# Kernel tuning notes

Hardware: AMD Instinct MI355X
Metric: run time of the kernel (lower is better)

## Reference

```python
import jax, jax.numpy as jnp
import numpy as np

N_NODES = 100000
N_EDGES = 1200000
IN_DIM, HID_DIM, LAT_DIM = 128, 64, 32


def gcn_conv(x, W, b, src, dst, n_nodes):
    # PyG GCNConv with add_self_loops=True, symmetric normalization.
    # src/dst already include self loops.
    h = x @ W  # [N, out]
    deg = jax.ops.segment_sum(jnp.ones_like(dst, dtype=h.dtype), dst,
                              num_segments=n_nodes)  # includes self loop -> >=1
    dinv = jax.lax.rsqrt(deg)
    norm = dinv[src] * dinv[dst]  # [E]
    msg = h[src] * norm[:, None]  # gather + scale, [E, out]
    out = jax.ops.segment_sum(msg, dst, num_segments=n_nodes)  # scatter-add
    return out + b


def setup_inputs() -> dict:
    key = jax.random.key(0)
    ks = jax.random.split(key, 9)
    x = jax.random.normal(ks[0], (N_NODES, IN_DIM), dtype=jnp.float32)
    edge_index = jax.random.randint(ks[1], (2, N_EDGES), 0, N_NODES, dtype=jnp.int32)
    s1 = 1.0 / np.sqrt(IN_DIM)
    s2 = 1.0 / np.sqrt(HID_DIM)
    W1 = jax.random.uniform(ks[2], (IN_DIM, HID_DIM), jnp.float32, -s1, s1)
    b1 = jnp.zeros((HID_DIM,), jnp.float32)
    Wm = jax.random.uniform(ks[3], (HID_DIM, LAT_DIM), jnp.float32, -s2, s2)
    bm = jnp.zeros((LAT_DIM,), jnp.float32)
    Wv = jax.random.uniform(ks[4], (HID_DIM, LAT_DIM), jnp.float32, -s2, s2)
    bv = jnp.zeros((LAT_DIM,), jnp.float32)
    noise = jax.random.normal(ks[5], (N_NODES, LAT_DIM), dtype=jnp.float32)
    return {"x": x, "edge_index": edge_index, "W1": W1, "b1": b1,
            "Wm": Wm, "bm": bm, "Wv": Wv, "bv": bv, "noise": noise}


def reference(x, edge_index, W1, b1, Wm, bm, Wv, bv, noise):
    n = x.shape[0]
    loops = jnp.arange(n, dtype=edge_index.dtype)
    src = jnp.concatenate([edge_index[0], loops])
    dst = jnp.concatenate([edge_index[1], loops])
    h = jnp.tanh(gcn_conv(x, W1, b1, src, dst, n))
    mean = gcn_conv(h, Wm, bm, src, dst, n)
    logvar = gcn_conv(h, Wv, bv, src, dst, n)
    z = noise * jnp.exp(0.5 * logvar) + mean
    return (z, mean, logvar)
```

## Files before the change

### kernel.cpp

```cpp
#include <hip/hip_runtime.h>
#include <math.h>

#define TILE 4096
#define CSHIFT 11
#define CMASK 2047
#define NCMAX 64

typedef __attribute__((ext_vector_type(8))) short bf16x8;
typedef __attribute__((ext_vector_type(4))) float f32x4;


__device__ __forceinline__ unsigned int pack_bf16(float a, float b) {
  unsigned int ua = __float_as_uint(a);
  ua += 0x7FFFu + ((ua >> 16) & 1u);
  unsigned int ub = __float_as_uint(b);
  ub += 0x7FFFu + ((ub >> 16) & 1u);
  return (ua >> 16) | (ub & 0xFFFF0000u);
}

__device__ __forceinline__ void add8(float* acc, uint4 hv) {
  unsigned int u[4] = {hv.x, hv.y, hv.z, hv.w};
#pragma unroll
  for (int i = 0; i < 4; ++i) {
    acc[2 * i]     += __uint_as_float(u[i] << 16);
    acc[2 * i + 1] += __uint_as_float(u[i] & 0xFFFF0000u);
  }
}

__device__ __forceinline__ void fma4(float4& acc, float s, const float4& w) {
  acc.x = fmaf(s, w.x, acc.x);
  acc.y = fmaf(s, w.y, acc.y);
  acc.z = fmaf(s, w.z, acc.z);
  acc.w = fmaf(s, w.w, acc.w);
}


__global__ void zero_kernel(int* __restrict__ p, int n) {
  int i = blockIdx.x * blockDim.x + threadIdx.x;
  if (i < n) p[i] = 0;
}

__global__ __launch_bounds__(256) void coarse_hist_kernel(const int* __restrict__ dst,
    int* __restrict__ ccnt, int e) {
  __shared__ int h[NCMAX];
  if (threadIdx.x < NCMAX) h[threadIdx.x] = 0;
  __syncthreads();
  for (int i = blockIdx.x * 256 + threadIdx.x; i < e; i += gridDim.x * 256)
    atomicAdd(&h[dst[i] >> CSHIFT], 1);
  __syncthreads();
  if (threadIdx.x < NCMAX && h[threadIdx.x])
    atomicAdd(&ccnt[threadIdx.x * 16], h[threadIdx.x]);
}

__global__ __launch_bounds__(64) void coarse_scan_kernel(const int* __restrict__ ccnt,
    int* __restrict__ coff, int* __restrict__ ccur, int* __restrict__ off,
    int nc, int n, int e) {
  int t = threadIdx.x;
  int v = (t < nc) ? ccnt[t * 16] : 0;
  int incl = v;
#pragma unroll
  for (int ofs = 1; ofs < 64; ofs <<= 1) {
    int w = __shfl_up(incl, ofs);
    if (t >= ofs) incl += w;
  }
  int excl = incl - v;
  if (t < nc) { coff[t] = excl; ccur[t * 16] = excl; }
  if (t == nc - 1) coff[nc] = incl;
  if (t == 0) off[n] = e;
}

__global__ __launch_bounds__(256) void coarse_partition_kernel(const int* __restrict__ src,
    const int* __restrict__ dst, int* __restrict__ ccur,
    unsigned int* __restrict__ packed, int e) {
  __shared__ unsigned int stage[TILE];
  __shared__ unsigned char bid[TILE];
  __shared__ int hist[NCMAX], excl[NCMAX], gbase[NCMAX], lcur[NCMAX];
  int ntiles = (e + TILE - 1) / TILE;
  for (int tile = blockIdx.x; tile < ntiles; tile += gridDim.x) {
    int i0 = tile * TILE;
    int cnt = e - i0; if (cnt > TILE) cnt = TILE;
    if (threadIdx.x < NCMAX) hist[threadIdx.x] = 0;
    __syncthreads();
    int myS[16], myD[16];
#pragma unroll
    for (int k = 0; k < 16; ++k) {
      int li = threadIdx.x + k * 256;
      if (li < cnt) {
        myS[k] = src[i0 + li];
        myD[k] = dst[i0 + li];
        atomicAdd(&hist[myD[k] >> CSHIFT], 1);
      }
    }
    __syncthreads();
    if (threadIdx.x < NCMAX) {
      int t = threadIdx.x;
      int v = hist[t];
      int incl = v;
#pragma unroll
      for (int ofs = 1; ofs < 64; ofs <<= 1) {
        int w = __shfl_up(incl, ofs);
        if (t >= ofs) incl += w;
      }
      excl[t] = incl - v;
      lcur[t] = incl - v;
    }
    __syncthreads();
#pragma unroll
    for (int k = 0; k < 16; ++k) {
      int li = threadIdx.x + k * 256;
      if (li < cnt) {
        int c = myD[k] >> CSHIFT;
        int p = atomicAdd(&lcur[c], 1);
        stage[p] = (unsigned int)myS[k] | ((unsigned int)(myD[k] & CMASK) << 17);
        bid[p] = (unsigned char)c;
      }
    }
    __syncthreads();
    if (threadIdx.x < NCMAX) {
      int t = threadIdx.x;
      int cc = lcur[t] - excl[t];
      gbase[t] = cc ? atomicAdd(&ccur[t * 16], cc) : 0;
    }
    __syncthreads();
    for (int i = threadIdx.x; i < cnt; i += 256) {
      int c = bid[i];
      packed[gbase[c] + (i - excl[c])] = stage[i];
    }
    __syncthreads();
  }
}

__global__ __launch_bounds__(512) void csr_fine_kernel(const unsigned int* __restrict__ packed,
    const int* __restrict__ coff, int* __restrict__ off, float* __restrict__ dinv,
    int* __restrict__ csr, int n) {
  __shared__ int lh[2048];
  __shared__ int lsum[512];
  int b = blockIdx.x;
  int t = threadIdx.x;
  int e0 = coff[b], e1 = coff[b + 1];
  int node0 = b << CSHIFT;
  for (int i = t; i < 2048; i += 512) lh[i] = 0;
  __syncthreads();
  for (int i = e0 + t; i < e1; i += 512) atomicAdd(&lh[packed[i] >> 17], 1);
  __syncthreads();
  int base = t * 4;
  int v0 = lh[base], v1 = lh[base + 1], v2 = lh[base + 2], v3 = lh[base + 3];
  int tsum = v0 + v1 + v2 + v3;
  lsum[t] = tsum;
  __syncthreads();
  for (int ofs = 1; ofs < 512; ofs <<= 1) {
    int add = (t >= ofs) ? lsum[t - ofs] : 0;
    __syncthreads();
    lsum[t] += add;
    __syncthreads();
  }
  int ex = lsum[t] - tsum;
  int exc0 = ex, exc1 = ex + v0, exc2 = ex + v0 + v1, exc3 = ex + v0 + v1 + v2;
  lh[base] = exc0; lh[base + 1] = exc1; lh[base + 2] = exc2; lh[base + 3] = exc3;
  int node = node0 + base;
  if (node < n)     { off[node]     = e0 + exc0; dinv[node]     = rsqrtf((float)(v0 + 1)); }
  if (node + 1 < n) { off[node + 1] = e0 + exc1; dinv[node + 1] = rsqrtf((float)(v1 + 1)); }
  if (node + 2 < n) { off[node + 2] = e0 + exc2; dinv[node + 2] = rsqrtf((float)(v2 + 1)); }
  if (node + 3 < n) { off[node + 3] = e0 + exc3; dinv[node + 3] = rsqrtf((float)(v3 + 1)); }
  __syncthreads();
  for (int i = e0 + t; i < e1; i += 512) {
    unsigned int p = packed[i];
    int nl = p >> 17;
    int pos = atomicAdd(&lh[nl], 1);
    csr[e0 + pos] = (int)(p & 0x1FFFFu);
  }
}

__global__ __launch_bounds__(256) void gemm1_kernel(const float* __restrict__ x,
    const float* __restrict__ W1, const float* __restrict__ dinv,
    unsigned int* __restrict__ h1, int n) {
  __shared__ unsigned int xs[64 * 64];
  __shared__ unsigned int wt[64 * 64];
  for (int i = threadIdx.x; i < 4096; i += 256) {
    int c = i & 63, kp = i >> 6;
    float a = W1[(2 * kp) * 64 + c];
    float b = W1[(2 * kp + 1) * 64 + c];
    int slot = kp >> 2;
    int slotS = slot ^ (c & 7);
    wt[c * 64 + slotS * 4 + (kp & 3)] = pack_bf16(a, b);
  }
  int row0 = blockIdx.x * 64;
  int nrow = n - row0; if (nrow > 64) nrow = 64;
  for (int i = threadIdx.x; i < 64 * 32; i += 256) {
    int r = i >> 5, q = i & 31;
    float4 v = make_float4(0.f, 0.f, 0.f, 0.f);
    if (r < nrow) v = ((const float4*)(x + (size_t)(row0 + r) * 128))[q];
    int slot = q >> 1;
    int slotS = slot ^ (r & 7);
    int bi = r * 64 + slotS * 4 + (q & 1) * 2;
    xs[bi]     = pack_bf16(v.x, v.y);
    xs[bi + 1] = pack_bf16(v.z, v.w);
  }
  __syncthreads();
  int lane = threadIdx.x & 63;
  int w = threadIdx.x >> 6;
  int rl = lane & 15;
  int g = lane >> 4;
  f32x4 acc[4];
#pragma unroll
  for (int i = 0; i < 4; ++i) acc[i] = (f32x4){0.f, 0.f, 0.f, 0.f};
#pragma unroll
  for (int ks = 0; ks < 4; ++ks) {
    int as = ((ks * 4 + g) ^ (rl & 7)) * 4;
    bf16x8 af = *reinterpret_cast<const bf16x8*>(&xs[(w * 16 + rl) * 64 + as]);
#pragma unroll
    for (int nt = 0; nt < 4; ++nt) {
      int col = nt * 16 + rl;
      int bs = ((ks * 4 + g) ^ (col & 7)) * 4;
      bf16x8 bfr = *reinterpret_cast<const bf16x8*>(&wt[col * 64 + bs]);
      acc[nt] = __builtin_amdgcn_mfma_f32_16x16x32_bf16(af, bfr, acc[nt], 0, 0, 0);
    }
  }
#pragma unroll
  for (int i = 0; i < 4; ++i) {
    int row = row0 + w * 16 + g * 4 + i;
    float dv = (row < n) ? dinv[row] : 0.f;
#pragma unroll
    for (int nt = 0; nt < 4; ++nt) {
      float val = dv * acc[nt][i];
      float pv = __shfl_xor(val, 1);
      if (!(lane & 1) && row < n) {
        h1[(size_t)row * 32 + nt * 8 + (rl >> 1)] = pack_bf16(val, pv);
      }
    }
  }
}

template <int EPI>
__global__ __launch_bounds__(256) void agg_kernel(const uint4* __restrict__ h4,
    const int* __restrict__ off, const int* __restrict__ csr,
    const float* __restrict__ dinv, const float* __restrict__ bias,
    unsigned int* __restrict__ out, int n) {
  int node = blockIdx.x * 4 + (threadIdx.x >> 6);
  if (node >= n) return;
  int lane = threadIdx.x & 63;
  int j = lane >> 2;
  int l = lane & 3;
  float acc[16];
#pragma unroll
  for (int i = 0; i < 16; ++i) acc[i] = 0.f;
  if (j == 0) {
    uint4 a = h4[(size_t)node * 8 + l * 2];
    uint4 b = h4[(size_t)node * 8 + l * 2 + 1];
    add8(acc, a);
    add8(acc + 8, b);
  }
  int e1 = off[node + 1];
  for (int ee = off[node] + j; ee < e1; ee += 16) {
    int s = __builtin_nontemporal_load(&csr[ee]);
    uint4 a = h4[(size_t)s * 8 + l * 2];
    uint4 b = h4[(size_t)s * 8 + l * 2 + 1];
    add8(acc, a);
    add8(acc + 8, b);
  }
#pragma unroll
  for (int i = 0; i < 8; ++i) {
    float tlo = acc[i]     + __shfl_xor(acc[i], 4);
    float thi = acc[i + 8] + __shfl_xor(acc[i + 8], 4);
    acc[i] = (j & 1) ? thi : tlo;
  }
#pragma unroll
  for (int i = 0; i < 4; ++i) {
    float tlo = acc[i]     + __shfl_xor(acc[i], 8);
    float thi = acc[i + 4] + __shfl_xor(acc[i + 4], 8);
    acc[i] = (j & 2) ? thi : tlo;
  }
#pragma unroll
  for (int i = 0; i < 2; ++i) {
    float tlo = acc[i]     + __shfl_xor(acc[i], 16);
    float thi = acc[i + 2] + __shfl_xor(acc[i + 2], 16);
    acc[i] = (j & 4) ? thi : tlo;
  }
  float a0, a1;
  a0 = acc[0] + __shfl_xor(acc[0], 32);
  a1 = acc[1] + __shfl_xor(acc[1], 32);
  float a = (j & 8) ? a1 : a0;
  int f = l * 16 + ((j & 1) << 3) + ((j & 2) << 1) + ((j >> 2) & 1) * 2 + ((j >> 3) & 1);
  float di = dinv[node];
  float val;
  if (EPI) {
    val = di * tanhf(fmaf(di, a, bias[f]));
  } else {
    val = di * a;
  }
  float pv = __shfl_xor(val, 32);
  if (!(j & 8)) {
    unsigned int w = pack_bf16(val, pv);
    int half = l * 8 + ((j & 1) << 2) + (j & 2) + ((j >> 2) & 1);
    out[(size_t)node * 32 + half] = w;
  }
}

__global__ __launch_bounds__(256) void final_kernel(const unsigned int* __restrict__ aggb,
    const float* __restrict__ Wm, const float* __restrict__ bm,
    const float* __restrict__ Wv, const float* __restrict__ bv,
    const float* __restrict__ noise, float* __restrict__ outZ,
    float* __restrict__ outM, float* __restrict__ outLv, int n) {
  __shared__ float WmS[64 * 32];
  __shared__ float WvS[64 * 32];
  __shared__ float aggS[64 * 68];
  for (int i = threadIdx.x; i < 64 * 8; i += 256) {
    ((float4*)WmS)[i] = ((const float4*)Wm)[i];
    ((float4*)WvS)[i] = ((const float4*)Wv)[i];
  }
  int row0 = blockIdx.x * 64;
  int nrow = n - row0; if (nrow > 64) nrow = 64;
  for (int i = threadIdx.x; i < 64 * 16; i += 256) {
    int r = i >> 4, g = i & 15;
    uint2 u = make_uint2(0u, 0u);
    if (r < nrow) u = ((const uint2*)aggb)[(size_t)(row0 + r) * 16 + g];
    float* d = &aggS[r * 68 + g * 4];
    d[0] = __uint_as_float(u.x << 16);
    d[1] = __uint_as_float(u.x & 0xFFFF0000u);
    d[2] = __uint_as_float(u.y << 16);
    d[3] = __uint_as_float(u.y & 0xFFFF0000u);
  }
  __syncthreads();
  int c4 = (threadIdx.x & 7) * 4;
  int r2 = (threadIdx.x >> 3) * 2;
  float4 am[2], av[2];
#pragma unroll
  for (int i = 0; i < 2; ++i) {
    am[i] = make_float4(0.f, 0.f, 0.f, 0.f);
    av[i] = make_float4(0.f, 0.f, 0.f, 0.f);
  }
#pragma unroll 4
  for (int kq = 0; kq < 16; ++kq) {
    float4 xa[2], wm[4], wv[4];
#pragma unroll
    for (int i = 0; i < 2; ++i) xa[i] = *(const float4*)&aggS[(r2 + i) * 68 + kq * 4];
#pragma unroll
    for (int q = 0; q < 4; ++q) {
      wm[q] = *(const float4*)&WmS[(kq * 4 + q) * 32 + c4];
      wv[q] = *(const float4*)&WvS[(kq * 4 + q) * 32 + c4];
    }
#pragma unroll
    for (int i = 0; i < 2; ++i) {
      fma4(am[i], xa[i].x, wm[0]); fma4(am[i], xa[i].y, wm[1]);
      fma4(am[i], xa[i].z, wm[2]); fma4(am[i], xa[i].w, wm[3]);
      fma4(av[i], xa[i].x, wv[0]); fma4(av[i], xa[i].y, wv[1]);
      fma4(av[i], xa[i].z, wv[2]); fma4(av[i], xa[i].w, wv[3]);
    }
  }
  float4 bmv = *(const float4*)&bm[c4];
  float4 bvv = *(const float4*)&bv[c4];
#pragma unroll
  for (int i = 0; i < 2; ++i) {
    int row = row0 + r2 + i;
    if (row < n) {
      float4 m = am[i]; m.x += bmv.x; m.y += bmv.y; m.z += bmv.z; m.w += bmv.w;
      float4 v = av[i]; v.x += bvv.x; v.y += bvv.y; v.z += bvv.z; v.w += bvv.w;
      size_t oi = (size_t)row * 8 + (threadIdx.x & 7);
      float4 nz = ((const float4*)noise)[oi];
      float4 z;
      z.x = fmaf(nz.x, expf(0.5f * v.x), m.x);
      z.y = fmaf(nz.y, expf(0.5f * v.y), m.y);
      z.z = fmaf(nz.z, expf(0.5f * v.z), m.z);
      z.w = fmaf(nz.w, expf(0.5f * v.w), m.w);
      ((float4*)outZ)[oi] = z;
      ((float4*)outM)[oi] = m;
      ((float4*)outLv)[oi] = v;
    }
  }
}


extern "C" void kernel_launch(void* const* d_in, const int* in_sizes, int n_in,
                              void* d_out, int out_size, void* d_ws, size_t ws_size,
                              hipStream_t stream) {
  const float* x     = (const float*)d_in[0];
  const int*   edge  = (const int*)d_in[1];
  const float* W1    = (const float*)d_in[2];
  const float* b1    = (const float*)d_in[3];
  const float* Wm    = (const float*)d_in[4];
  const float* bm    = (const float*)d_in[5];
  const float* Wv    = (const float*)d_in[6];
  const float* bv    = (const float*)d_in[7];
  const float* noise = (const float*)d_in[8];
  int n = in_sizes[0] / 128;
  int e = in_sizes[1] / 2;
  const int* src = edge;
  const int* dst = edge + e;
  int nc = (n + CMASK) >> CSHIFT;

  int* ccnt = (int*)d_ws;
  int* ccur = ccnt + NCMAX * 16;
  int* coff = ccur + NCMAX * 16;
  int* off  = coff + (NCMAX + 4);
  float* dinv = (float*)(off + ((n + 4) & ~3));
  unsigned int* packed = (unsigned int*)(dinv + ((n + 3) & ~3));
  int* csr  = (int*)(packed + ((e + 3) & ~3));
  unsigned int* h1b = (unsigned int*)(csr + ((e + 3) & ~3));
  unsigned int* hb  = h1b + (size_t)n * 32;
  unsigned int* aggb = hb + (size_t)n * 32;

  float* outZ  = (float*)d_out;
  float* outM  = outZ + (size_t)n * 32;
  float* outLv = outM + (size_t)n * 32;

  int ntiles = (e + TILE - 1) / TILE;

  zero_kernel<<<(NCMAX * 16 + 255) / 256, 256, 0, stream>>>(ccnt, NCMAX * 16);
  coarse_hist_kernel<<<256, 256, 0, stream>>>(dst, ccnt, e);
  coarse_scan_kernel<<<1, 64, 0, stream>>>(ccnt, coff, ccur, off, nc, n, e);
  coarse_partition_kernel<<<ntiles, 256, 0, stream>>>(src, dst, ccur, packed, e);
  csr_fine_kernel<<<nc, 512, 0, stream>>>(packed, coff, off, dinv, csr, n);
  gemm1_kernel<<<(n + 63) / 64, 256, 0, stream>>>(x, W1, dinv, h1b, n);
  agg_kernel<1><<<(n + 3) / 4, 256, 0, stream>>>((const uint4*)h1b, off, csr, dinv, b1, hb, n);
  agg_kernel<0><<<(n + 3) / 4, 256, 0, stream>>>((const uint4*)hb, off, csr, dinv, b1, aggb, n);
  final_kernel<<<(n + 63) / 64, 256, 0, stream>>>(aggb, Wm, bm, Wv, bv, noise, outZ, outM, outLv, n);
}
```

Measured before the change: 195.6 us.

## Process two nodes per wavefront in aggregation with wider per-lane loads

The aggregation kernel now maps two nodes to each 64-lane wavefront, with 32 lanes per node: 16 edge slots times 2 feature halves. Each lane loads 64 bytes (four uint4) per edge instead of 32, and the butterfly reduction gains an extra shuffle stage. This targets wasted lanes on low-degree nodes (average degree about 13) and issues more memory requests per lane. The cost is 32 accumulator registers per lane, which may lower occupancy, plus one more reduction stage.

```diff
diff --git a/kernel.cpp b/kernel.cpp
--- a/kernel.cpp
+++ b/kernel.cpp
@@ -236,63 +236,66 @@
     const int* __restrict__ off, const int* __restrict__ csr,
     const float* __restrict__ dinv, const float* __restrict__ bias,
     unsigned int* __restrict__ out, int n) {
-  int node = blockIdx.x * 4 + (threadIdx.x >> 6);
-  if (node >= n) return;
   int lane = threadIdx.x & 63;
-  int j = lane >> 2;
-  int l = lane & 3;
-  float acc[16];
-#pragma unroll
-  for (int i = 0; i < 16; ++i) acc[i] = 0.f;
-  if (j == 0) {
-    uint4 a = h4[(size_t)node * 8 + l * 2];
-    uint4 b = h4[(size_t)node * 8 + l * 2 + 1];
-    add8(acc, a);
-    add8(acc + 8, b);
-  }
-  int e1 = off[node + 1];
-  for (int ee = off[node] + j; ee < e1; ee += 16) {
-    int s = __builtin_nontemporal_load(&csr[ee]);
-    uint4 a = h4[(size_t)s * 8 + l * 2];
-    uint4 b = h4[(size_t)s * 8 + l * 2 + 1];
-    add8(acc, a);
-    add8(acc + 8, b);
+  int nd = lane >> 5;
+  int j  = (lane >> 1) & 15;
+  int fl = lane & 1;
+  int node = blockIdx.x * 8 + (threadIdx.x >> 6) * 2 + nd;
+  bool valid = node < n;
+  float acc[32];
+#pragma unroll
+  for (int i = 0; i < 32; ++i) acc[i] = 0.f;
+  if (valid) {
+    if (j == 0) {
+      const uint4* hp = &h4[(size_t)node * 8 + fl * 4];
+      uint4 a = hp[0], b = hp[1], c = hp[2], d = hp[3];
+      add8(acc, a); add8(acc + 8, b); add8(acc + 16, c); add8(acc + 24, d);
+    }
+    int e1 = off[node + 1];
+    for (int ee = off[node] + j; ee < e1; ee += 16) {
+      int s = __builtin_nontemporal_load(&csr[ee]);
+      const uint4* hp = &h4[(size_t)s * 8 + fl * 4];
+      uint4 a = hp[0], b = hp[1], c = hp[2], d = hp[3];
+      add8(acc, a); add8(acc + 8, b); add8(acc + 16, c); add8(acc + 24, d);
+    }
+  }
+#pragma unroll
+  for (int i = 0; i < 16; ++i) {
+    float tlo = acc[i]      + __shfl_xor(acc[i], 2);
+    float thi = acc[i + 16] + __shfl_xor(acc[i + 16], 2);
+    acc[i] = (j & 1) ? thi : tlo;
   }
 #pragma unroll
   for (int i = 0; i < 8; ++i) {
     float tlo = acc[i]     + __shfl_xor(acc[i], 4);
     float thi = acc[i + 8] + __shfl_xor(acc[i + 8], 4);
-    acc[i] = (j & 1) ? thi : tlo;
+    acc[i] = (j & 2) ? thi : tlo;
   }
 #pragma unroll
   for (int i = 0; i < 4; ++i) {
     float tlo = acc[i]     + __shfl_xor(acc[i], 8);
     float thi = acc[i + 4] + __shfl_xor(acc[i + 4], 8);
-    acc[i] = (j & 2) ? thi : tlo;
+    acc[i] = (j & 4) ? thi : tlo;
   }
 #pragma unroll
   for (int i = 0; i < 2; ++i) {
     float tlo = acc[i]     + __shfl_xor(acc[i], 16);
     float thi = acc[i + 2] + __shfl_xor(acc[i + 2], 16);
-    acc[i] = (j & 4) ? thi : tlo;
-  }
-  float a0, a1;
-  a0 = acc[0] + __shfl_xor(acc[0], 32);
-  a1 = acc[1] + __shfl_xor(acc[1], 32);
-  float a = (j & 8) ? a1 : a0;
-  int f = l * 16 + ((j & 1) << 3) + ((j & 2) << 1) + ((j >> 2) & 1) * 2 + ((j >> 3) & 1);
-  float di = dinv[node];
-  float val;
-  if (EPI) {
-    val = di * tanhf(fmaf(di, a, bias[f]));
-  } else {
-    val = di * a;
-  }
-  float pv = __shfl_xor(val, 32);
-  if (!(j & 8)) {
-    unsigned int w = pack_bf16(val, pv);
-    int half = l * 8 + ((j & 1) << 2) + (j & 2) + ((j >> 2) & 1);
-    out[(size_t)node * 32 + half] = w;
+    acc[i] = (j & 8) ? thi : tlo;
+  }
+  int b0 = j & 1, b1 = (j >> 1) & 1, b2 = (j >> 2) & 1, b3 = (j >> 3) & 1;
+  int f0 = fl * 32 + 16 * b0 + 8 * b1 + 4 * b2 + 2 * b3;
+  if (valid) {
+    float di = dinv[node];
+    float v0, v1;
+    if (EPI) {
+      v0 = di * tanhf(fmaf(di, acc[0], bias[f0]));
+      v1 = di * tanhf(fmaf(di, acc[1], bias[f0 + 1]));
+    } else {
+      v0 = di * acc[0];
+      v1 = di * acc[1];
+    }
+    out[(size_t)node * 32 + (f0 >> 1)] = pack_bf16(v0, v1);
   }
 }
 
@@ -411,7 +414,7 @@
   coarse_partition_kernel<<<ntiles, 256, 0, stream>>>(src, dst, ccur, packed, e);
   csr_fine_kernel<<<nc, 512, 0, stream>>>(packed, coff, off, dinv, csr, n);
   gemm1_kernel<<<(n + 63) / 64, 256, 0, stream>>>(x, W1, dinv, h1b, n);
-  agg_kernel<1><<<(n + 3) / 4, 256, 0, stream>>>((const uint4*)h1b, off, csr, dinv, b1, hb, n);
-  agg_kernel<0><<<(n + 3) / 4, 256, 0, stream>>>((const uint4*)hb, off, csr, dinv, b1, aggb, n);
+  agg_kernel<1><<<(n + 7) / 8, 256, 0, stream>>>((const uint4*)h1b, off, csr, dinv, b1, hb, n);
+  agg_kernel<0><<<(n + 7) / 8, 256, 0, stream>>>((const uint4*)hb, off, csr, dinv, b1, aggb, n);
   final_kernel<<<(n + 63) / 64, 256, 0, stream>>>(aggb, Wm, bm, Wv, bv, noise, outZ, outM, outLv, n);
 }
```

Result: no change. 192.8 us (-1.4%).
